# Kernel optimization log

Hardware: AMD Instinct MI355X
Metric: run time of the kernel (lower is better)

The kernel has to match this reference:

```python
import jax, jax.numpy as jnp
import numpy as np
from jax.scipy.special import logsumexp

IMP = -10000.0  # penalty value used by init_crf_transitions


def _make_params():
    # BIO tag set with 10 entity types, matching init_kwargs tag_names
    names = ["O"] + [f"{p}-T{k}" for k in range(1, 11) for p in ("B", "I")]
    T = len(names)
    rng = np.random.default_rng(0)
    start = rng.uniform(-0.1, 0.1, T).astype(np.float32)
    end = rng.uniform(-0.1, 0.1, T).astype(np.float32)
    trans = rng.uniform(-0.1, 0.1, (T, T)).astype(np.float32)
    pre = [n.split("-")[0] for n in names]
    ent = [n.split("-")[1] if "-" in n else "" for n in names]
    for i in range(T):
        if pre[i] in ("B", "I"):  # invalid_begin / invalid_end for BIO
            start[i] = IMP
            end[i] = IMP
        for j in range(T):
            if pre[i] == "O" and pre[j] == "I":  # O -> I invalid
                trans[i, j] = IMP
            if pre[i] in ("B", "I") and pre[j] == "I" and ent[i] != ent[j]:
                trans[i, j] = IMP  # B-x/I-x -> I-y invalid when x != y
    return jnp.asarray(start), jnp.asarray(end), jnp.asarray(trans), T


def setup_inputs() -> dict:
    key = jax.random.key(0)
    k1, k2 = jax.random.split(key)
    start, end, trans, T = _make_params()
    B, L = 1024, 1024
    emissions = jax.random.normal(k1, (B, L, T), dtype=jnp.float32)
    tags = jax.random.randint(k2, (B, L), 0, T)
    mask = jnp.ones((B, L), dtype=bool)  # torchcrf requires mask[:, 0] all on
    return {
        "emissions": emissions,
        "tags": tags,
        "mask": mask,
        "start_transitions": start,
        "end_transitions": end,
        "transitions": trans,
    }


def _crf_llh(emissions, tags, mask, start, end, trans):
    # batch_first=True: convert to time-major like torchcrf does internally
    em = jnp.swapaxes(emissions, 0, 1)   # [L, B, T]
    tg = jnp.swapaxes(tags, 0, 1)        # [L, B]
    mk = jnp.swapaxes(mask, 0, 1)        # [L, B] bool
    mkf = mk.astype(em.dtype)
    L, B, T = em.shape

    # --- numerator: score of the gold tag sequence ---
    em_sc = jnp.take_along_axis(em, tg[..., None], axis=2)[..., 0]  # [L, B]
    score = start[tg[0]] + em_sc[0]
    tr_sc = trans[tg[:-1], tg[1:]]  # [L-1, B]
    score = score + ((tr_sc + em_sc[1:]) * mkf[1:]).sum(axis=0)
    last_idx = mkf.sum(axis=0).astype(jnp.int32) - 1  # seq end per batch
    last_tags = tg[last_idx, jnp.arange(B)]
    score = score + end[last_tags]

    # --- denominator: log-partition via forward algorithm (scan) ---
    def step(alpha, xs):
        e_i, m_i = xs  # e_i: [B, T], m_i: [B] bool
        nxt = logsumexp(alpha[:, :, None] + trans[None, :, :] + e_i[:, None, :], axis=1)
        return jnp.where(m_i[:, None], nxt, alpha), None

    alpha0 = start[None, :] + em[0]  # [B, T]
    alpha, _ = jax.lax.scan(step, alpha0, (em[1:], mk[1:]))
    denom = logsumexp(alpha + end[None, :], axis=1)  # [B]

    return score - denom  # per-sequence log-likelihood


def reference(emissions, tags, mask, start_transitions, end_transitions, transitions):
    llh = _crf_llh(emissions, tags, mask, start_transitions, end_transitions, transitions)
    # reduction='token_mean'
    return llh.sum() / mask.astype(emissions.dtype).sum()
```

## Files before the change

kernel.cpp:

```cpp
#include <hip/hip_runtime.h>


#define TT 21
#define BB 1024
#define LL 1024

__device__ __forceinline__ float rdlane(float v, int lane) {
    return __int_as_float(__builtin_amdgcn_readlane(__float_as_int(v), lane));
}

__device__ __forceinline__ float matvec21(float q, const float (&e)[TT]) {
    float a0 = 0.f, a1 = 0.f, a2 = 0.f;
#pragma unroll
    for (int t = 0; t < TT; t += 3) {
        a0 = fmaf(rdlane(q, t + 0), e[t + 0], a0);
        a1 = fmaf(rdlane(q, t + 1), e[t + 1], a1);
        a2 = fmaf(rdlane(q, t + 2), e[t + 2], a2);
    }
    return (a0 + a1) + a2;
}

__device__ __forceinline__ void rescale(float& v, float& s) {
    const float m = rdlane(v, 0);
    const unsigned u = __float_as_uint(m);
    const int bi = (int)((u >> 23) & 0xFFu);
    s += (float)(bi - 127) * 0.69314718056f;
    v *= __uint_as_float((unsigned)(254 - bi) << 23);
}

#define ISSUE8_ASC(r0,r1,r2,r3,r4,r5,r6,r7, base) do { \
    asm volatile("global_load_dword %0, %1, off"            : "=v"(r0) : "v"(base)); \
    asm volatile("global_load_dword %0, %1, off offset:84"  : "=v"(r1) : "v"(base)); \
    asm volatile("global_load_dword %0, %1, off offset:168" : "=v"(r2) : "v"(base)); \
    asm volatile("global_load_dword %0, %1, off offset:252" : "=v"(r3) : "v"(base)); \
    asm volatile("global_load_dword %0, %1, off offset:336" : "=v"(r4) : "v"(base)); \
    asm volatile("global_load_dword %0, %1, off offset:420" : "=v"(r5) : "v"(base)); \
    asm volatile("global_load_dword %0, %1, off offset:504" : "=v"(r6) : "v"(base)); \
    asm volatile("global_load_dword %0, %1, off offset:588" : "=v"(r7) : "v"(base)); \
} while (0)

#define ISSUE8_DESC(r0,r1,r2,r3,r4,r5,r6,r7, base) do { \
    asm volatile("global_load_dword %0, %1, off offset:588" : "=v"(r0) : "v"(base)); \
    asm volatile("global_load_dword %0, %1, off offset:504" : "=v"(r1) : "v"(base)); \
    asm volatile("global_load_dword %0, %1, off offset:420" : "=v"(r2) : "v"(base)); \
    asm volatile("global_load_dword %0, %1, off offset:336" : "=v"(r3) : "v"(base)); \
    asm volatile("global_load_dword %0, %1, off offset:252" : "=v"(r4) : "v"(base)); \
    asm volatile("global_load_dword %0, %1, off offset:168" : "=v"(r5) : "v"(base)); \
    asm volatile("global_load_dword %0, %1, off offset:84"  : "=v"(r6) : "v"(base)); \
    asm volatile("global_load_dword %0, %1, off"            : "=v"(r7) : "v"(base)); \
} while (0)

#define WAIT8(r0,r1,r2,r3,r4,r5,r6,r7) \
    asm volatile("s_waitcnt vmcnt(8)" \
                 : "+v"(r0), "+v"(r1), "+v"(r2), "+v"(r3), \
                   "+v"(r4), "+v"(r5), "+v"(r6), "+v"(r7))

#define DRAIN16(a0,a1,a2,a3,a4,a5,a6,a7,b0,b1,b2,b3,b4,b5,b6,b7) \
    asm volatile("s_waitcnt vmcnt(0)" \
                 : "+v"(a0), "+v"(a1), "+v"(a2), "+v"(a3), \
                   "+v"(a4), "+v"(a5), "+v"(a6), "+v"(a7), \
                   "+v"(b0), "+v"(b1), "+v"(b2), "+v"(b3), \
                   "+v"(b4), "+v"(b5), "+v"(b6), "+v"(b7))

#define WS_QV 0
#define WS_WV (BB * 32)
#define WS_SF (2 * BB * 32)
#define WS_SB (WS_SF + BB)
#define WS_SP (WS_SB + BB)

__global__ __launch_bounds__(256) void crf_chain_k(
    const float* __restrict__ em,
    const int* __restrict__ tags,
    const float* __restrict__ startv,
    const float* __restrict__ endv,
    const float* __restrict__ trans,
    float* __restrict__ ws)
{
    const int tid  = threadIdx.x;
    const int wave = tid >> 6;
    const int j    = tid & 63;
    const bool act = (j < TT);
    const int  jc  = act ? j : (TT - 1);
    const bool fwd = (blockIdx.x < 256);
    const int  b   = (fwd ? blockIdx.x : (blockIdx.x - 256)) * 4 + wave;

    {
        const int* tg = tags + (size_t)b * LL;
        const float* emB = em + (size_t)b * LL * TT;
        float p = 0.0f;
        if (fwd) {
            if (j == 0) { const int t0 = tg[0]; p = startv[t0] + emB[t0]; }
#pragma unroll
            for (int m = 0; m < 8; ++m) {
                const int i = 1 + j + 64 * m;
                const int tp = tg[i - 1];
                const int tc = tg[i];
                p += trans[tp * TT + tc] + emB[(size_t)i * TT + tc];
            }
        } else {
#pragma unroll
            for (int m = 0; m < 8; ++m) {
                const int i = 513 + j + 64 * m;
                if (i < LL) {
                    const int tp = tg[i - 1];
                    const int tc = tg[i];
                    p += trans[tp * TT + tc] + emB[(size_t)i * TT + tc];
                    if (i == LL - 1) p += endv[tc];
                }
            }
        }
        for (int o = 32; o > 0; o >>= 1) p += __shfl_down(p, o, 64);
        if (j == 0) ws[WS_SP + b * 2 + (fwd ? 0 : 1)] = p;
    }

    const float* emb = em + (size_t)b * LL * TT + jc;

    if (fwd) {
        float e[TT];
#pragma unroll
        for (int t = 0; t < TT; ++t) {
            float tv = trans[t * TT + jc];
            e[t] = act ? __expf(tv) : 0.0f;
        }
        float q = act ? __expf(startv[jc] + emb[0]) : 0.0f;
        float s = 0.0f;

        float a0,a1,a2,a3,a4,a5,a6,a7, b0,b1,b2,b3,b4,b5,b6,b7;
        asm volatile("s_waitcnt vmcnt(0)");
        const float* pA = emb + (size_t)1 * TT;
        const float* pB = emb + (size_t)9 * TT;
        ISSUE8_ASC(a0,a1,a2,a3,a4,a5,a6,a7, pA);
        ISSUE8_ASC(b0,b1,b2,b3,b4,b5,b6,b7, pB);
        pA += 16 * TT;
        pB += 16 * TT;

        for (int it = 0; it < 32; ++it) {
            WAIT8(a0,a1,a2,a3,a4,a5,a6,a7);
            {
                const float x0=__expf(a0), x1=__expf(a1), x2=__expf(a2), x3=__expf(a3);
                const float x4=__expf(a4), x5=__expf(a5), x6=__expf(a6), x7=__expf(a7);
                ISSUE8_ASC(a0,a1,a2,a3,a4,a5,a6,a7, pA);
                pA += 16 * TT;
                q = matvec21(q, e) * x0;
                q = matvec21(q, e) * x1;
                q = matvec21(q, e) * x2;
                q = matvec21(q, e) * x3;
                q = matvec21(q, e) * x4;
                q = matvec21(q, e) * x5;
                q = matvec21(q, e) * x6;
                q = matvec21(q, e) * x7;
                rescale(q, s);
            }
            WAIT8(b0,b1,b2,b3,b4,b5,b6,b7);
            {
                const float x0=__expf(b0), x1=__expf(b1), x2=__expf(b2), x3=__expf(b3);
                const float x4=__expf(b4), x5=__expf(b5), x6=__expf(b6), x7=__expf(b7);
                ISSUE8_ASC(b0,b1,b2,b3,b4,b5,b6,b7, pB);
                pB += 16 * TT;
                q = matvec21(q, e) * x0;
                q = matvec21(q, e) * x1;
                q = matvec21(q, e) * x2;
                q = matvec21(q, e) * x3;
                q = matvec21(q, e) * x4;
                q = matvec21(q, e) * x5;
                q = matvec21(q, e) * x6;
                q = matvec21(q, e) * x7;
                rescale(q, s);
            }
        }
        DRAIN16(a0,a1,a2,a3,a4,a5,a6,a7, b0,b1,b2,b3,b4,b5,b6,b7);

        if (j < 32) ws[WS_QV + b * 32 + j] = act ? q : 0.0f;
        if (j == 0) ws[WS_SF + b] = s;
    } else {
        float er[TT];
#pragma unroll
        for (int t = 0; t < TT; ++t) {
            float tv = trans[jc * TT + t];
            er[t] = act ? __expf(tv) : 0.0f;
        }
        float w = act ? __expf(endv[jc]) : 0.0f;
        float s = 0.0f;

        float a0,a1,a2,a3,a4,a5,a6,a7, b0,b1,b2,b3,b4,b5,b6,b7;
        asm volatile("s_waitcnt vmcnt(0)");
        const float* pA = emb + (size_t)1016 * TT;
        const float* pB = emb + (size_t)1008 * TT;
        ISSUE8_DESC(a0,a1,a2,a3,a4,a5,a6,a7, pA);
        ISSUE8_DESC(b0,b1,b2,b3,b4,b5,b6,b7, pB);
        pA -= 16 * TT;
        pB -= 16 * TT;

        for (int it = 0; it < 31; ++it) {
            WAIT8(a0,a1,a2,a3,a4,a5,a6,a7);
            {
                const float x0=__expf(a0), x1=__expf(a1), x2=__expf(a2), x3=__expf(a3);
                const float x4=__expf(a4), x5=__expf(a5), x6=__expf(a6), x7=__expf(a7);
                ISSUE8_DESC(a0,a1,a2,a3,a4,a5,a6,a7, pA);
                pA -= 16 * TT;
                w = matvec21(w * x0, er);
                w = matvec21(w * x1, er);
                w = matvec21(w * x2, er);
                w = matvec21(w * x3, er);
                w = matvec21(w * x4, er);
                w = matvec21(w * x5, er);
                w = matvec21(w * x6, er);
                w = matvec21(w * x7, er);
                rescale(w, s);
            }
            WAIT8(b0,b1,b2,b3,b4,b5,b6,b7);
            {
                const float x0=__expf(b0), x1=__expf(b1), x2=__expf(b2), x3=__expf(b3);
                const float x4=__expf(b4), x5=__expf(b5), x6=__expf(b6), x7=__expf(b7);
                ISSUE8_DESC(b0,b1,b2,b3,b4,b5,b6,b7, pB);
                pB -= 16 * TT;
                w = matvec21(w * x0, er);
                w = matvec21(w * x1, er);
                w = matvec21(w * x2, er);
                w = matvec21(w * x3, er);
                w = matvec21(w * x4, er);
                w = matvec21(w * x5, er);
                w = matvec21(w * x6, er);
                w = matvec21(w * x7, er);
                rescale(w, s);
            }
        }
        WAIT8(a0,a1,a2,a3,a4,a5,a6,a7);
        {
            const float x0=__expf(a0), x1=__expf(a1), x2=__expf(a2), x3=__expf(a3);
            const float x4=__expf(a4), x5=__expf(a5), x6=__expf(a6), x7=__expf(a7);
            w = matvec21(w * x0, er);
            w = matvec21(w * x1, er);
            w = matvec21(w * x2, er);
            w = matvec21(w * x3, er);
            w = matvec21(w * x4, er);
            w = matvec21(w * x5, er);
            w = matvec21(w * x6, er);
            w = matvec21(w * x7, er);
            rescale(w, s);
        }
        DRAIN16(a0,a1,a2,a3,a4,a5,a6,a7, b0,b1,b2,b3,b4,b5,b6,b7);
        w = matvec21(w * __expf(b0), er);
        w = matvec21(w * __expf(b1), er);
        w = matvec21(w * __expf(b2), er);
        w = matvec21(w * __expf(b3), er);
        w = matvec21(w * __expf(b4), er);
        w = matvec21(w * __expf(b5), er);
        w = matvec21(w * __expf(b6), er);

        if (j < 32) ws[WS_WV + b * 32 + j] = act ? w : 0.0f;
        if (j == 0) ws[WS_SB + b] = s;
    }
}

__global__ __launch_bounds__(1024) void crf_final_k(
    const float* __restrict__ ws,
    float* __restrict__ out)
{
    const int t = threadIdx.x;

    float dot = 0.0f;
#pragma unroll
    for (int tt = 0; tt < TT; ++tt)
        dot += ws[WS_QV + t * 32 + tt] * ws[WS_WV + t * 32 + tt];

    const float denom = ws[WS_SF + t] + ws[WS_SB + t] + __logf(dot);
    const float sc = ws[WS_SP + t * 2 + 0] + ws[WS_SP + t * 2 + 1];
    float v = sc - denom;

    for (int o = 32; o > 0; o >>= 1) v += __shfl_down(v, o, 64);
    __shared__ float red[16];
    if ((t & 63) == 0) red[t >> 6] = v;
    __syncthreads();
    if (t < 16) {
        float w = red[t];
        w += __shfl_down(w, 8, 16);
        w += __shfl_down(w, 4, 16);
        w += __shfl_down(w, 2, 16);
        w += __shfl_down(w, 1, 16);
        if (t == 0) out[0] = w * (1.0f / ((float)BB * (float)LL));
    }
}

extern "C" void kernel_launch(void* const* d_in, const int* in_sizes, int n_in,
                              void* d_out, int out_size, void* d_ws, size_t ws_size,
                              hipStream_t stream) {
    const float* em     = (const float*)d_in[0];
    const int*   tags   = (const int*)d_in[1];
    const float* startv = (const float*)d_in[3];
    const float* endv   = (const float*)d_in[4];
    const float* trans  = (const float*)d_in[5];

    float* ws  = (float*)d_ws;
    float* out = (float*)d_out;

    crf_chain_k<<<512, 256, 0, stream>>>(em, tags, startv, endv, trans, ws);
    crf_final_k<<<1, 1024, 0, stream>>>(ws, out);
}
```

Baseline: 232.2 us.

## Pack two sequences per wavefront using ds_bpermute half-wave broadcasts

Each 64-lane wave now carries two batch sequences, one per 32-lane half. This halves the number of waves and blocks (256 instead of 512). Because the two halves need different source lanes, the readlane broadcasts in the matvec and rescale steps are replaced with ds_bpermute using per-half address tables. The goal is to double useful lane utilisation, but bpermute goes through the LDS crossbar and has higher latency than readlane on the serial recurrence chain. The inactive lanes 21-31 now write their values unmasked into the workspace.

```diff
diff --git a/kernel.cpp b/kernel.cpp
--- a/kernel.cpp
+++ b/kernel.cpp
@@ -5,23 +5,27 @@
 #define BB 1024
 #define LL 1024
 
-__device__ __forceinline__ float rdlane(float v, int lane) {
-    return __int_as_float(__builtin_amdgcn_readlane(__float_as_int(v), lane));
-}
-
-__device__ __forceinline__ float matvec21(float q, const float (&e)[TT]) {
+__device__ __forceinline__ float bperm(int adr, float v) {
+    return __int_as_float(__builtin_amdgcn_ds_bpermute(adr, __float_as_int(v)));
+}
+
+__device__ __forceinline__ float matvec2(float q, const float (&e)[TT],
+                                         const int (&adr)[TT]) {
     float a0 = 0.f, a1 = 0.f, a2 = 0.f;
 #pragma unroll
     for (int t = 0; t < TT; t += 3) {
-        a0 = fmaf(rdlane(q, t + 0), e[t + 0], a0);
-        a1 = fmaf(rdlane(q, t + 1), e[t + 1], a1);
-        a2 = fmaf(rdlane(q, t + 2), e[t + 2], a2);
+        const float b0 = bperm(adr[t + 0], q);
+        const float b1 = bperm(adr[t + 1], q);
+        const float b2 = bperm(adr[t + 2], q);
+        a0 = fmaf(b0, e[t + 0], a0);
+        a1 = fmaf(b1, e[t + 1], a1);
+        a2 = fmaf(b2, e[t + 2], a2);
     }
     return (a0 + a1) + a2;
 }
 
-__device__ __forceinline__ void rescale(float& v, float& s) {
-    const float m = rdlane(v, 0);
+__device__ __forceinline__ void rescale2(float& v, float& s, int adr0) {
+    const float m = bperm(adr0, v);
     const unsigned u = __float_as_uint(m);
     const int bi = (int)((u >> 23) & 0xFFu);
     s += (float)(bi - 127) * 0.69314718056f;
@@ -78,29 +82,36 @@
 {
     const int tid  = threadIdx.x;
     const int wave = tid >> 6;
-    const int j    = tid & 63;
+    const int lane = tid & 63;
+    const int j    = lane & 31;
+    const int hi   = lane >> 5;
     const bool act = (j < TT);
     const int  jc  = act ? j : (TT - 1);
-    const bool fwd = (blockIdx.x < 256);
-    const int  b   = (fwd ? blockIdx.x : (blockIdx.x - 256)) * 4 + wave;
+    const bool fwd = (blockIdx.x < 128);
+    const int  bb  = (fwd ? blockIdx.x : (blockIdx.x - 128)) * 8 + wave * 2 + hi;
+
+    int adr[TT];
+#pragma unroll
+    for (int t = 0; t < TT; ++t) adr[t] = ((lane & 32) + t) * 4;
+    const int adr0 = (lane & 32) * 4;
 
     {
-        const int* tg = tags + (size_t)b * LL;
-        const float* emB = em + (size_t)b * LL * TT;
+        const int* tg = tags + (size_t)bb * LL;
+        const float* emB = em + (size_t)bb * LL * TT;
         float p = 0.0f;
         if (fwd) {
             if (j == 0) { const int t0 = tg[0]; p = startv[t0] + emB[t0]; }
 #pragma unroll
-            for (int m = 0; m < 8; ++m) {
-                const int i = 1 + j + 64 * m;
+            for (int m = 0; m < 16; ++m) {
+                const int i = 1 + j + 32 * m;
                 const int tp = tg[i - 1];
                 const int tc = tg[i];
                 p += trans[tp * TT + tc] + emB[(size_t)i * TT + tc];
             }
         } else {
 #pragma unroll
-            for (int m = 0; m < 8; ++m) {
-                const int i = 513 + j + 64 * m;
+            for (int m = 0; m < 16; ++m) {
+                const int i = 513 + j + 32 * m;
                 if (i < LL) {
                     const int tp = tg[i - 1];
                     const int tc = tg[i];
@@ -109,11 +120,11 @@
                 }
             }
         }
-        for (int o = 32; o > 0; o >>= 1) p += __shfl_down(p, o, 64);
-        if (j == 0) ws[WS_SP + b * 2 + (fwd ? 0 : 1)] = p;
+        for (int o = 16; o > 0; o >>= 1) p += __shfl_down(p, o, 32);
+        if (j == 0) ws[WS_SP + bb * 2 + (fwd ? 0 : 1)] = p;
     }
 
-    const float* emb = em + (size_t)b * LL * TT + jc;
+    const float* emb = em + (size_t)bb * LL * TT + jc;
 
     if (fwd) {
         float e[TT];
@@ -141,15 +152,15 @@
                 const float x4=__expf(a4), x5=__expf(a5), x6=__expf(a6), x7=__expf(a7);
                 ISSUE8_ASC(a0,a1,a2,a3,a4,a5,a6,a7, pA);
                 pA += 16 * TT;
-                q = matvec21(q, e) * x0;
-                q = matvec21(q, e) * x1;
-                q = matvec21(q, e) * x2;
-                q = matvec21(q, e) * x3;
-                q = matvec21(q, e) * x4;
-                q = matvec21(q, e) * x5;
-                q = matvec21(q, e) * x6;
-                q = matvec21(q, e) * x7;
-                rescale(q, s);
+                q = matvec2(q, e, adr) * x0;
+                q = matvec2(q, e, adr) * x1;
+                q = matvec2(q, e, adr) * x2;
+                q = matvec2(q, e, adr) * x3;
+                q = matvec2(q, e, adr) * x4;
+                q = matvec2(q, e, adr) * x5;
+                q = matvec2(q, e, adr) * x6;
+                q = matvec2(q, e, adr) * x7;
+                rescale2(q, s, adr0);
             }
             WAIT8(b0,b1,b2,b3,b4,b5,b6,b7);
             {
@@ -157,21 +168,21 @@
                 const float x4=__expf(b4), x5=__expf(b5), x6=__expf(b6), x7=__expf(b7);
                 ISSUE8_ASC(b0,b1,b2,b3,b4,b5,b6,b7, pB);
                 pB += 16 * TT;
-                q = matvec21(q, e) * x0;
-                q = matvec21(q, e) * x1;
-                q = matvec21(q, e) * x2;
-                q = matvec21(q, e) * x3;
-                q = matvec21(q, e) * x4;
-                q = matvec21(q, e) * x5;
-                q = matvec21(q, e) * x6;
-                q = matvec21(q, e) * x7;
-                rescale(q, s);
+                q = matvec2(q, e, adr) * x0;
+                q = matvec2(q, e, adr) * x1;
+                q = matvec2(q, e, adr) * x2;
+                q = matvec2(q, e, adr) * x3;
+                q = matvec2(q, e, adr) * x4;
+                q = matvec2(q, e, adr) * x5;
+                q = matvec2(q, e, adr) * x6;
+                q = matvec2(q, e, adr) * x7;
+                rescale2(q, s, adr0);
             }
         }
         DRAIN16(a0,a1,a2,a3,a4,a5,a6,a7, b0,b1,b2,b3,b4,b5,b6,b7);
 
-        if (j < 32) ws[WS_QV + b * 32 + j] = act ? q : 0.0f;
-        if (j == 0) ws[WS_SF + b] = s;
+        ws[WS_QV + bb * 32 + j] = q;
+        if (j == 0) ws[WS_SF + bb] = s;
     } else {
         float er[TT];
 #pragma unroll
@@ -198,15 +209,15 @@
                 const float x4=__expf(a4), x5=__expf(a5), x6=__expf(a6), x7=__expf(a7);
                 ISSUE8_DESC(a0,a1,a2,a3,a4,a5,a6,a7, pA);
                 pA -= 16 * TT;
-                w = matvec21(w * x0, er);
-                w = matvec21(w * x1, er);
-                w = matvec21(w * x2, er);
-                w = matvec21(w * x3, er);
-                w = matvec21(w * x4, er);
-                w = matvec21(w * x5, er);
-                w = matvec21(w * x6, er);
-                w = matvec21(w * x7, er);
-                rescale(w, s);
+                w = matvec2(w * x0, er, adr);
+                w = matvec2(w * x1, er, adr);
+                w = matvec2(w * x2, er, adr);
+                w = matvec2(w * x3, er, adr);
+                w = matvec2(w * x4, er, adr);
+                w = matvec2(w * x5, er, adr);
+                w = matvec2(w * x6, er, adr);
+                w = matvec2(w * x7, er, adr);
+                rescale2(w, s, adr0);
             }
             WAIT8(b0,b1,b2,b3,b4,b5,b6,b7);
             {
@@ -214,42 +225,42 @@
                 const float x4=__expf(b4), x5=__expf(b5), x6=__expf(b6), x7=__expf(b7);
                 ISSUE8_DESC(b0,b1,b2,b3,b4,b5,b6,b7, pB);
                 pB -= 16 * TT;
-                w = matvec21(w * x0, er);
-                w = matvec21(w * x1, er);
-                w = matvec21(w * x2, er);
-                w = matvec21(w * x3, er);
-                w = matvec21(w * x4, er);
-                w = matvec21(w * x5, er);
-                w = matvec21(w * x6, er);
-                w = matvec21(w * x7, er);
-                rescale(w, s);
+                w = matvec2(w * x0, er, adr);
+                w = matvec2(w * x1, er, adr);
+                w = matvec2(w * x2, er, adr);
+                w = matvec2(w * x3, er, adr);
+                w = matvec2(w * x4, er, adr);
+                w = matvec2(w * x5, er, adr);
+                w = matvec2(w * x6, er, adr);
+                w = matvec2(w * x7, er, adr);
+                rescale2(w, s, adr0);
             }
         }
         WAIT8(a0,a1,a2,a3,a4,a5,a6,a7);
         {
             const float x0=__expf(a0), x1=__expf(a1), x2=__expf(a2), x3=__expf(a3);
             const float x4=__expf(a4), x5=__expf(a5), x6=__expf(a6), x7=__expf(a7);
-            w = matvec21(w * x0, er);
-            w = matvec21(w * x1, er);
-            w = matvec21(w * x2, er);
-            w = matvec21(w * x3, er);
-            w = matvec21(w * x4, er);
-            w = matvec21(w * x5, er);
-            w = matvec21(w * x6, er);
-            w = matvec21(w * x7, er);
-            rescale(w, s);
+            w = matvec2(w * x0, er, adr);
+            w = matvec2(w * x1, er, adr);
+            w = matvec2(w * x2, er, adr);
+            w = matvec2(w * x3, er, adr);
+            w = matvec2(w * x4, er, adr);
+            w = matvec2(w * x5, er, adr);
+            w = matvec2(w * x6, er, adr);
+            w = matvec2(w * x7, er, adr);
+            rescale2(w, s, adr0);
         }
         DRAIN16(a0,a1,a2,a3,a4,a5,a6,a7, b0,b1,b2,b3,b4,b5,b6,b7);
-        w = matvec21(w * __expf(b0), er);
-        w = matvec21(w * __expf(b1), er);
-        w = matvec21(w * __expf(b2), er);
-        w = matvec21(w * __expf(b3), er);
-        w = matvec21(w * __expf(b4), er);
-        w = matvec21(w * __expf(b5), er);
-        w = matvec21(w * __expf(b6), er);
-
-        if (j < 32) ws[WS_WV + b * 32 + j] = act ? w : 0.0f;
-        if (j == 0) ws[WS_SB + b] = s;
+        w = matvec2(w * __expf(b0), er, adr);
+        w = matvec2(w * __expf(b1), er, adr);
+        w = matvec2(w * __expf(b2), er, adr);
+        w = matvec2(w * __expf(b3), er, adr);
+        w = matvec2(w * __expf(b4), er, adr);
+        w = matvec2(w * __expf(b5), er, adr);
+        w = matvec2(w * __expf(b6), er, adr);
+
+        ws[WS_WV + bb * 32 + j] = w;
+        if (j == 0) ws[WS_SB + bb] = s;
     }
 }
 
@@ -294,6 +305,6 @@
     float* ws  = (float*)d_ws;
     float* out = (float*)d_out;
 
-    crf_chain_k<<<512, 256, 0, stream>>>(em, tags, startv, endv, trans, ws);
+    crf_chain_k<<<256, 256, 0, stream>>>(em, tags, startv, endv, trans, ws);
     crf_final_k<<<1, 1024, 0, stream>>>(ws, out);
 }
```

Result: slower. 307.0 us (+32.2%).

## Replace readlane matvec with bf16 packed dot2 via ds_bpermute broadcast

Applied to the files above, without the earlier changes.

Each recurrence step now packs neighbouring lane pairs of the state into bf16 using a DPP swap. It broadcasts the 11 packed pairs with ds_bpermute and accumulates using v_dot2_f32_bf16 against bf16-packed exp(transition) weights. This replaces 21 scalar readlanes and FMAs per step with 11 permutes and 11 dot2 ops, aiming to shorten the serial dependency chain. It lowers precision of both the state and the weights to bf16 at every step, which may accumulate error over 1024 steps. It also adds LDS-permute latency plus a full lgkmcnt wait on the critical path.

```diff
diff --git a/kernel.cpp b/kernel.cpp
--- a/kernel.cpp
+++ b/kernel.cpp
@@ -9,15 +9,57 @@
     return __int_as_float(__builtin_amdgcn_readlane(__float_as_int(v), lane));
 }
 
-__device__ __forceinline__ float matvec21(float q, const float (&e)[TT]) {
+__device__ __forceinline__ float dpp_swap1(float v) {
+    return __int_as_float(__builtin_amdgcn_mov_dpp(__float_as_int(v), 0xB1, 0xF, 0xF, true));
+}
+
+__device__ __forceinline__ unsigned pack_bf16(float lo, float hi) {
+    const unsigned ul = __float_as_uint(lo) + 0x8000u;
+    const unsigned uh = __float_as_uint(hi) + 0x8000u;
+    return __builtin_amdgcn_perm(uh, ul, 0x07060302u);
+}
+
+#define DOT2(acc, qp, ev) \
+    asm("v_dot2_f32_bf16 %0, %1, %2, %0" : "+v"(acc) : "v"(qp), "v"(ev))
+
+__device__ __forceinline__ float pair_dot(unsigned pk, const unsigned (&ep)[11],
+                                          const int (&adr)[11]) {
+    int r0,r1,r2,r3,r4,r5,r6,r7,r8,r9,r10;
+    asm volatile("ds_bpermute_b32 %0, %1, %2" : "=v"(r0)  : "v"(adr[0]),  "v"(pk));
+    asm volatile("ds_bpermute_b32 %0, %1, %2" : "=v"(r1)  : "v"(adr[1]),  "v"(pk));
+    asm volatile("ds_bpermute_b32 %0, %1, %2" : "=v"(r2)  : "v"(adr[2]),  "v"(pk));
+    asm volatile("ds_bpermute_b32 %0, %1, %2" : "=v"(r3)  : "v"(adr[3]),  "v"(pk));
+    asm volatile("ds_bpermute_b32 %0, %1, %2" : "=v"(r4)  : "v"(adr[4]),  "v"(pk));
+    asm volatile("ds_bpermute_b32 %0, %1, %2" : "=v"(r5)  : "v"(adr[5]),  "v"(pk));
+    asm volatile("ds_bpermute_b32 %0, %1, %2" : "=v"(r6)  : "v"(adr[6]),  "v"(pk));
+    asm volatile("ds_bpermute_b32 %0, %1, %2" : "=v"(r7)  : "v"(adr[7]),  "v"(pk));
+    asm volatile("ds_bpermute_b32 %0, %1, %2" : "=v"(r8)  : "v"(adr[8]),  "v"(pk));
+    asm volatile("ds_bpermute_b32 %0, %1, %2" : "=v"(r9)  : "v"(adr[9]),  "v"(pk));
+    asm volatile("ds_bpermute_b32 %0, %1, %2" : "=v"(r10) : "v"(adr[10]), "v"(pk));
+    asm volatile("s_waitcnt lgkmcnt(0)"
+                 : "+v"(r0), "+v"(r1), "+v"(r2), "+v"(r3), "+v"(r4), "+v"(r5),
+                   "+v"(r6), "+v"(r7), "+v"(r8), "+v"(r9), "+v"(r10));
     float a0 = 0.f, a1 = 0.f, a2 = 0.f;
-#pragma unroll
-    for (int t = 0; t < TT; t += 3) {
-        a0 = fmaf(rdlane(q, t + 0), e[t + 0], a0);
-        a1 = fmaf(rdlane(q, t + 1), e[t + 1], a1);
-        a2 = fmaf(rdlane(q, t + 2), e[t + 2], a2);
-    }
+    DOT2(a0, r0, ep[0]);  DOT2(a1, r1, ep[1]);  DOT2(a2, r2,  ep[2]);
+    DOT2(a0, r3, ep[3]);  DOT2(a1, r4, ep[4]);  DOT2(a2, r5,  ep[5]);
+    DOT2(a0, r6, ep[6]);  DOT2(a1, r7, ep[7]);  DOT2(a2, r8,  ep[8]);
+    DOT2(a0, r9, ep[9]);  DOT2(a1, r10, ep[10]);
     return (a0 + a1) + a2;
+}
+
+__device__ __forceinline__ float fwd_step(float q, float x, const unsigned (&ep)[11],
+                                          const int (&adr)[11]) {
+    const float nb = dpp_swap1(q);
+    const unsigned pk = pack_bf16(q, nb);
+    return pair_dot(pk, ep, adr) * x;
+}
+
+__device__ __forceinline__ float bwd_step(float w, float x, const unsigned (&erp)[11],
+                                          const int (&adr)[11]) {
+    const float u = w * x;
+    const float nb = dpp_swap1(u);
+    const unsigned pk = pack_bf16(u, nb);
+    return pair_dot(pk, erp, adr);
 }
 
 __device__ __forceinline__ void rescale(float& v, float& s) {
@@ -115,12 +157,18 @@
 
     const float* emb = em + (size_t)b * LL * TT + jc;
 
+    int adr[11];
+#pragma unroll
+    for (int t = 0; t < 11; ++t) adr[t] = 8 * t;
+
     if (fwd) {
-        float e[TT];
-#pragma unroll
-        for (int t = 0; t < TT; ++t) {
-            float tv = trans[t * TT + jc];
-            e[t] = act ? __expf(tv) : 0.0f;
+        unsigned ep[11];
+#pragma unroll
+        for (int t = 0; t < 11; ++t) {
+            const float lo = act ? __expf(trans[(2 * t) * TT + jc]) : 0.0f;
+            const float hi = (act && (2 * t + 1 < TT))
+                             ? __expf(trans[(2 * t + 1) * TT + jc]) : 0.0f;
+            ep[t] = pack_bf16(lo, hi);
         }
         float q = act ? __expf(startv[jc] + emb[0]) : 0.0f;
         float s = 0.0f;
@@ -141,14 +189,14 @@
                 const float x4=__expf(a4), x5=__expf(a5), x6=__expf(a6), x7=__expf(a7);
                 ISSUE8_ASC(a0,a1,a2,a3,a4,a5,a6,a7, pA);
                 pA += 16 * TT;
-                q = matvec21(q, e) * x0;
-                q = matvec21(q, e) * x1;
-                q = matvec21(q, e) * x2;
-                q = matvec21(q, e) * x3;
-                q = matvec21(q, e) * x4;
-                q = matvec21(q, e) * x5;
-                q = matvec21(q, e) * x6;
-                q = matvec21(q, e) * x7;
+                q = fwd_step(q, x0, ep, adr);
+                q = fwd_step(q, x1, ep, adr);
+                q = fwd_step(q, x2, ep, adr);
+                q = fwd_step(q, x3, ep, adr);
+                q = fwd_step(q, x4, ep, adr);
+                q = fwd_step(q, x5, ep, adr);
+                q = fwd_step(q, x6, ep, adr);
+                q = fwd_step(q, x7, ep, adr);
                 rescale(q, s);
             }
             WAIT8(b0,b1,b2,b3,b4,b5,b6,b7);
@@ -157,14 +205,14 @@
                 const float x4=__expf(b4), x5=__expf(b5), x6=__expf(b6), x7=__expf(b7);
                 ISSUE8_ASC(b0,b1,b2,b3,b4,b5,b6,b7, pB);
                 pB += 16 * TT;
-                q = matvec21(q, e) * x0;
-                q = matvec21(q, e) * x1;
-                q = matvec21(q, e) * x2;
-                q = matvec21(q, e) * x3;
-                q = matvec21(q, e) * x4;
-                q = matvec21(q, e) * x5;
-                q = matvec21(q, e) * x6;
-                q = matvec21(q, e) * x7;
+                q = fwd_step(q, x0, ep, adr);
+                q = fwd_step(q, x1, ep, adr);
+                q = fwd_step(q, x2, ep, adr);
+                q = fwd_step(q, x3, ep, adr);
+                q = fwd_step(q, x4, ep, adr);
+                q = fwd_step(q, x5, ep, adr);
+                q = fwd_step(q, x6, ep, adr);
+                q = fwd_step(q, x7, ep, adr);
                 rescale(q, s);
             }
         }
@@ -173,11 +221,13 @@
         if (j < 32) ws[WS_QV + b * 32 + j] = act ? q : 0.0f;
         if (j == 0) ws[WS_SF + b] = s;
     } else {
-        float er[TT];
-#pragma unroll
-        for (int t = 0; t < TT; ++t) {
-            float tv = trans[jc * TT + t];
-            er[t] = act ? __expf(tv) : 0.0f;
+        unsigned erp[11];
+#pragma unroll
+        for (int t = 0; t < 11; ++t) {
+            const float lo = act ? __expf(trans[jc * TT + 2 * t]) : 0.0f;
+            const float hi = (act && (2 * t + 1 < TT))
+                             ? __expf(trans[jc * TT + 2 * t + 1]) : 0.0f;
+            erp[t] = pack_bf16(lo, hi);
         }
         float w = act ? __expf(endv[jc]) : 0.0f;
         float s = 0.0f;
@@ -198,14 +248,14 @@
                 const float x4=__expf(a4), x5=__expf(a5), x6=__expf(a6), x7=__expf(a7);
                 ISSUE8_DESC(a0,a1,a2,a3,a4,a5,a6,a7, pA);
                 pA -= 16 * TT;
-                w = matvec21(w * x0, er);
-                w = matvec21(w * x1, er);
-                w = matvec21(w * x2, er);
-                w = matvec21(w * x3, er);
-                w = matvec21(w * x4, er);
-                w = matvec21(w * x5, er);
-                w = matvec21(w * x6, er);
-                w = matvec21(w * x7, er);
+                w = bwd_step(w, x0, erp, adr);
+                w = bwd_step(w, x1, erp, adr);
+                w = bwd_step(w, x2, erp, adr);
+                w = bwd_step(w, x3, erp, adr);
+                w = bwd_step(w, x4, erp, adr);
+                w = bwd_step(w, x5, erp, adr);
+                w = bwd_step(w, x6, erp, adr);
+                w = bwd_step(w, x7, erp, adr);
                 rescale(w, s);
             }
             WAIT8(b0,b1,b2,b3,b4,b5,b6,b7);
@@ -214,14 +264,14 @@
                 const float x4=__expf(b4), x5=__expf(b5), x6=__expf(b6), x7=__expf(b7);
                 ISSUE8_DESC(b0,b1,b2,b3,b4,b5,b6,b7, pB);
                 pB -= 16 * TT;
-                w = matvec21(w * x0, er);
-                w = matvec21(w * x1, er);
-                w = matvec21(w * x2, er);
-                w = matvec21(w * x3, er);
-                w = matvec21(w * x4, er);
-                w = matvec21(w * x5, er);
-                w = matvec21(w * x6, er);
-                w = matvec21(w * x7, er);
+                w = bwd_step(w, x0, erp, adr);
+                w = bwd_step(w, x1, erp, adr);
+                w = bwd_step(w, x2, erp, adr);
+                w = bwd_step(w, x3, erp, adr);
+                w = bwd_step(w, x4, erp, adr);
+                w = bwd_step(w, x5, erp, adr);
+                w = bwd_step(w, x6, erp, adr);
+                w = bwd_step(w, x7, erp, adr);
                 rescale(w, s);
             }
         }
@@ -229,24 +279,24 @@
         {
             const float x0=__expf(a0), x1=__expf(a1), x2=__expf(a2), x3=__expf(a3);
             const float x4=__expf(a4), x5=__expf(a5), x6=__expf(a6), x7=__expf(a7);
-            w = matvec21(w * x0, er);
-            w = matvec21(w * x1, er);
-            w = matvec21(w * x2, er);
-            w = matvec21(w * x3, er);
-            w = matvec21(w * x4, er);
-            w = matvec21(w * x5, er);
-            w = matvec21(w * x6, er);
-            w = matvec21(w * x7, er);
+            w = bwd_step(w, x0, erp, adr);
+            w = bwd_step(w, x1, erp, adr);
+            w = bwd_step(w, x2, erp, adr);
+            w = bwd_step(w, x3, erp, adr);
+            w = bwd_step(w, x4, erp, adr);
+            w = bwd_step(w, x5, erp, adr);
+            w = bwd_step(w, x6, erp, adr);
+            w = bwd_step(w, x7, erp, adr);
             rescale(w, s);
         }
         DRAIN16(a0,a1,a2,a3,a4,a5,a6,a7, b0,b1,b2,b3,b4,b5,b6,b7);
-        w = matvec21(w * __expf(b0), er);
-        w = matvec21(w * __expf(b1), er);
-        w = matvec21(w * __expf(b2), er);
-        w = matvec21(w * __expf(b3), er);
-        w = matvec21(w * __expf(b4), er);
-        w = matvec21(w * __expf(b5), er);
-        w = matvec21(w * __expf(b6), er);
+        w = bwd_step(w, __expf(b0), erp, adr);
+        w = bwd_step(w, __expf(b1), erp, adr);
+        w = bwd_step(w, __expf(b2), erp, adr);
+        w = bwd_step(w, __expf(b3), erp, adr);
+        w = bwd_step(w, __expf(b4), erp, adr);
+        w = bwd_step(w, __expf(b5), erp, adr);
+        w = bwd_step(w, __expf(b6), erp, adr);
 
         if (j < 32) ws[WS_WV + b * 32 + j] = act ? w : 0.0f;
         if (j == 0) ws[WS_SB + b] = s;
```

New measurement: 275.5 us. 1.19x slower.
